# Optimization experiments

Hardware: AMD Instinct MI355X
Metric: run time of the kernel (lower is better)

## Reference

```python
import jax, jax.numpy as jnp
import numpy as np
import math

D_MODEL = 512
N_HEADS = 8
C = 1

def setup_inputs() -> dict:
    key = jax.random.key(0)
    ks = jax.random.split(key, 7)
    B, L, D = 4, 2048, 512
    f = lambda k, s: jax.random.normal(k, s, dtype=jnp.float32)
    return {
        "queries": f(ks[0], (B, L, D)),
        "keys": f(ks[1], (B, L, D)),
        "values": f(ks[2], (B, L, D)),
        "wq": f(ks[3], (D, D_MODEL)) * (1.0 / math.sqrt(D)),
        "wk": f(ks[4], (D, D_MODEL)) * (1.0 / math.sqrt(D)),
        "wv": f(ks[5], (D, D_MODEL)) * (1.0 / math.sqrt(D)),
        "wo": f(ks[6], (D_MODEL, D_MODEL)) * (1.0 / math.sqrt(D_MODEL)),
    }

def reference(queries, keys, values, wq, wk, wv, wo):
    B, Lq, _ = queries.shape
    Lk = keys.shape[1]
    H = N_HEADS
    Dh = D_MODEL // N_HEADS
    # projections -> [B,H,L,Dh]
    Q = (queries @ wq).reshape(B, Lq, H, Dh).transpose(0, 2, 1, 3)
    K = (keys @ wk).reshape(B, Lk, H, Dh).transpose(0, 2, 1, 3)
    V = (values @ wv).reshape(B, Lk, H, Dh).transpose(0, 2, 1, 3)
    # NOTE: original computes rfft/irfft correlation then OVERWRITES it with
    # this dense einsum; FFT branch is dead code and omitted here.
    corr = jnp.einsum('bhid,bhjd->bhij', Q, K)  # [B,H,Lq,Lk]
    # k derived from values.shape[3] == d_head in the original (quirk preserved)
    k = max(1, min(int(C * math.log(Dh)), Dh))
    mean_corr = corr.mean(axis=(1, 2))  # [B, Lk]
    top_vals, top_idx = jax.lax.top_k(mean_corr, k)  # [B,k]
    w = jax.nn.softmax(top_vals, axis=-1)  # [B,k]
    # rolled[b,j,h,l,d] = V[b,h,(l + delay[b,j]) % Lk, d]  (tf.roll with shift=-delay)
    idx = (jnp.arange(Lk)[None, None, :] + top_idx[:, :, None]) % Lk  # [B,k,Lk]
    gathered = jnp.take_along_axis(V[:, None], idx[:, :, None, :, None], axis=3)  # [B,k,H,Lk,Dh]
    agg = jnp.einsum('bk,bkhld->bhld', w, gathered)  # [B,H,Lk,Dh]
    # original: transpose (0,3,1,2) then reshape -> [B, Lq, d_model]
    out = agg.transpose(0, 3, 1, 2).reshape(B, Lq, D_MODEL)
    return out @ wo
```

## Files before the change

kernel.cpp:

```cpp
#include <hip/hip_runtime.h>
#include <hip/hip_bf16.h>
#include <float.h>
#include <math.h>

#define B  4
#define L  2048
#define D  512
#define K4 4

typedef __attribute__((ext_vector_type(8))) short  bf16x8;
typedef __attribute__((ext_vector_type(4))) float  f32x4;

#define VMIXB_OFF  0u
#define TT_OFF     8388608u
#define WVT_OFF    16777216u
#define WOT_OFF    17301504u
#define QPART_OFF  17825792u
#define TPART_OFF  18350080u
#define U_OFF      18415616u
#define SC_OFF     18423808u

static __device__ __forceinline__ unsigned short f2b(float f) {
    __hip_bfloat16 h = __float2bfloat16(f);
    return *reinterpret_cast<unsigned short*>(&h);
}

__global__ __launch_bounds__(256) void k_prep1(const float* __restrict__ q,
                                               const float* __restrict__ wv, const float* __restrict__ wo,
                                               float* __restrict__ qpart,
                                               unsigned short* __restrict__ wvT, unsigned short* __restrict__ woT) {
    __shared__ float s[32][33];
    int bid = blockIdx.x, tid = threadIdx.x;
    if (bid < 128) {
        int b = bid >> 5, lc = bid & 31;
        int c4 = tid & 127, half = tid >> 7;
        const float4* p = (const float4*)q + ((size_t)b * L + lc * 64 + half * 32) * 128 + c4;
        float4 a = make_float4(0.f, 0.f, 0.f, 0.f);
#pragma unroll 8
        for (int l = 0; l < 32; ++l) {
            float4 x = p[(size_t)l * 128];
            a.x += x.x; a.y += x.y; a.z += x.z; a.w += x.w;
        }
        ((float4*)qpart)[((b * 64) + lc * 2 + half) * 128 + c4] = a;
    } else {
        int id2 = bid - 128;
        int c0 = (id2 >> 4) * 32, n0 = (id2 & 15) * 32;
        int col = tid & 31, r8 = tid >> 5;
        for (int z = 0; z < 2; ++z) {
            const float* src = z ? wo : wv;
            unsigned short* dst = z ? woT : wvT;
#pragma unroll
            for (int rr = 0; rr < 4; ++rr) {
                int r = rr * 8 + r8;
                s[r][col] = src[(size_t)(c0 + r) * D + n0 + col];
            }
            __syncthreads();
#pragma unroll
            for (int rr = 0; rr < 4; ++rr) {
                int r = rr * 8 + r8;
                dst[(size_t)(n0 + r) * D + c0 + col] = f2b(s[col][r]);
            }
            __syncthreads();
        }
    }
}

__global__ void k_tpart(const float* __restrict__ wq, const float* __restrict__ qpart,
                        float* __restrict__ tpart) {
    __shared__ float part[256];
    __shared__ float qs[64];
    int b = blockIdx.x, jc = blockIdx.y, tid = threadIdx.x;
    int jj = tid & 63, cg = tid >> 6;
    float p = 0.f;
#pragma unroll
    for (int c = cg * 16; c < cg * 16 + 16; ++c)
        p += qpart[((b * 64) + c) * D + jc * 64 + jj];
    part[tid] = p;
    __syncthreads();
    if (tid < 64) qs[tid] = part[tid] + part[tid + 64] + part[tid + 128] + part[tid + 192];
    __syncthreads();
    float a0 = 0.f, a1 = 0.f;
#pragma unroll 8
    for (int j = 0; j < 64; ++j) {
        const float* wr = wq + (size_t)(jc * 64 + j) * D;
        float qv = qs[j];
        a0 += wr[tid] * qv;
        a1 += wr[tid + 256] * qv;
    }
    tpart[((b * 8) + jc) * D + tid] = a0;
    tpart[((b * 8) + jc) * D + tid + 256] = a1;
}

__global__ void k_uvec(const float* __restrict__ wk, const float* __restrict__ tpart,
                       float* __restrict__ u) {
    __shared__ __align__(16) float ts[D];
    int b = blockIdx.x, tid = threadIdx.x;
    for (int d = tid; d < D; d += 256) {
        float s = 0.f;
#pragma unroll
        for (int c = 0; c < 8; ++c) s += tpart[((b * 8) + c) * D + d];
        ts[d] = s;
    }
    __syncthreads();
    int wave = tid >> 6, lane = tid & 63;
    const float4* wk4 = (const float4*)wk;
    float4 t0 = *(const float4*)&ts[lane * 4];
    float4 t1 = *(const float4*)&ts[256 + lane * 4];
#pragma unroll
    for (int rr = 0; rr < 4; ++rr) {
        int i = blockIdx.y * 16 + wave * 4 + rr;
        float4 w0 = wk4[(size_t)i * 128 + lane];
        float4 w1 = wk4[(size_t)i * 128 + 64 + lane];
        float acc = w0.x * t0.x + w0.y * t0.y + w0.z * t0.z + w0.w * t0.w
                  + w1.x * t1.x + w1.y * t1.y + w1.z * t1.z + w1.w * t1.w;
        for (int m = 32; m; m >>= 1) acc += __shfl_xor(acc, m, 64);
        if (lane == 0) u[b * D + i] = acc * (1.f / 16384.f);
    }
}

__global__ void k_scores(const float* __restrict__ keys, const float* __restrict__ u,
                         float* __restrict__ sc) {
    __shared__ __align__(16) float us[D];
    int b = blockIdx.x, tid = threadIdx.x;
    for (int d = tid; d < D; d += 256) us[d] = u[b * D + d];
    __syncthreads();
    int wave = tid >> 6, lane = tid & 63;
    int j = blockIdx.y * 4 + wave;
    const float4* kp = (const float4*)(keys + ((size_t)b * L + j) * D);
    float4 u0 = *(const float4*)&us[lane * 4];
    float4 u1 = *(const float4*)&us[256 + lane * 4];
    float4 x0 = kp[lane], x1 = kp[lane + 64];
    float acc = x0.x * u0.x + x0.y * u0.y + x0.z * u0.z + x0.w * u0.w
              + x1.x * u1.x + x1.y * u1.y + x1.z * u1.z + x1.w * u1.w;
    for (int m = 32; m; m >>= 1) acc += __shfl_xor(acc, m, 64);
    if (lane == 0) sc[b * L + j] = acc;
}

__global__ __launch_bounds__(256) void k_vmixb(const float* __restrict__ values,
                                               const float* __restrict__ sc,
                                               uint4* __restrict__ vmixb) {
    __shared__ float sv[L];
    __shared__ float wv4[4]; __shared__ int wi4[4];
    __shared__ float wsh[K4]; __shared__ int ish[K4];
    int tid = threadIdx.x;
    int wave = tid >> 6, lane = tid & 63;
    int b = (int)(blockIdx.x >> 9);
    for (int i = tid; i < L; i += 256) sv[i] = sc[b * L + i];
    __syncthreads();
    float topv[K4]; int topi[K4];
    for (int it = 0; it < K4; ++it) {
        float bv = -FLT_MAX;
        int bi = 0x7fffffff;
#pragma unroll
        for (int i = 0; i < 8; ++i) {
            int idx = tid + i * 256;
            float v = sv[idx];
            if (v > bv) { bv = v; bi = idx; }
        }
        for (int m = 32; m; m >>= 1) {
            float v2 = __shfl_xor(bv, m, 64);
            int i2 = __shfl_xor(bi, m, 64);
            if (v2 > bv || (v2 == bv && i2 < bi)) { bv = v2; bi = i2; }
        }
        if (lane == 0) { wv4[wave] = bv; wi4[wave] = bi; }
        __syncthreads();
        float mv = wv4[0]; int mi = wi4[0];
#pragma unroll
        for (int w = 1; w < 4; ++w)
            if (wv4[w] > mv || (wv4[w] == mv && wi4[w] < mi)) { mv = wv4[w]; mi = wi4[w]; }
        topv[it] = mv; topi[it] = mi;
        if (tid == 0) sv[mi] = -FLT_MAX;
        __syncthreads();
    }
    if (tid == 0) {
        float mx = topv[0];
#pragma unroll
        for (int i = 1; i < K4; ++i) mx = fmaxf(mx, topv[i]);
        float ssum = 0.f, e[K4];
#pragma unroll
        for (int i = 0; i < K4; ++i) { e[i] = expf(topv[i] - mx); ssum += e[i]; }
#pragma unroll
        for (int i = 0; i < K4; ++i) { wsh[i] = e[i] / ssum; ish[i] = topi[i]; }
    }
    __syncthreads();

    size_t t = (size_t)blockIdx.x * 256 + tid;
    int l  = (int)((t >> 6) & (L - 1));
    int g8 = (int)(t & 63);
    const float4* vp = (const float4*)values;
    float4 r0 = make_float4(0.f, 0.f, 0.f, 0.f), r1 = r0;
#pragma unroll
    for (int j = 0; j < K4; ++j) {
        int ls = (l + ish[j]) & (L - 1);
        const float4* p = vp + ((size_t)b * L + ls) * 128 + g8 * 2;
        float4 x0 = p[0], x1 = p[1];
        float w = wsh[j];
        r0.x += w * x0.x; r0.y += w * x0.y; r0.z += w * x0.z; r0.w += w * x0.w;
        r1.x += w * x1.x; r1.y += w * x1.y; r1.z += w * x1.z; r1.w += w * x1.w;
    }
    uint4 o;
    o.x = (unsigned)f2b(r0.x) | ((unsigned)f2b(r0.y) << 16);
    o.y = (unsigned)f2b(r0.z) | ((unsigned)f2b(r0.w) << 16);
    o.z = (unsigned)f2b(r1.x) | ((unsigned)f2b(r1.y) << 16);
    o.w = (unsigned)f2b(r1.z) | ((unsigned)f2b(r1.w) << 16);
    vmixb[t] = o;
}

__global__ __launch_bounds__(256) void k_gemm1(const unsigned short* __restrict__ A,
                                               const unsigned short* __restrict__ Bt,
                                               unsigned short* __restrict__ Tt) {
    __shared__ __align__(16) unsigned short As[2][128][40];
    __shared__ __align__(16) unsigned short Bs[2][64][40];
    int m0 = blockIdx.x * 128, n0 = blockIdx.y * 64;
    int tid = threadIdx.x;
    int wave = tid >> 6, lane = tid & 63;
    int wr = wave >> 1, wc = wave & 1;
    int lr = lane & 15, lg = lane >> 4;
    f32x4 acc[4][2];
#pragma unroll
    for (int i = 0; i < 4; ++i)
#pragma unroll
        for (int j = 0; j < 2; ++j) acc[i][j] = (f32x4){0.f, 0.f, 0.f, 0.f};

    int aR = tid >> 1, aC = (tid & 1) * 16;
    int bR = tid >> 2, bC = (tid & 3) * 8;
    const unsigned short* Ap = A + (size_t)(m0 + aR) * D + aC;
    const unsigned short* Bp = Bt + (size_t)(n0 + bR) * D + bC;
    {
        uint4 va0 = *(const uint4*)(Ap);
        uint4 va1 = *(const uint4*)(Ap + 8);
        uint4 vb  = *(const uint4*)(Bp);
        *(uint4*)&As[0][aR][aC]     = va0;
        *(uint4*)&As[0][aR][aC + 8] = va1;
        *(uint4*)&Bs[0][bR][bC]     = vb;
    }
    __syncthreads();
    int cur = 0;
    for (int t = 0; t < 15; ++t) {
        int k0 = (t + 1) * 32;
        uint4 va0 = *(const uint4*)(Ap + k0);
        uint4 va1 = *(const uint4*)(Ap + k0 + 8);
        uint4 vb  = *(const uint4*)(Bp + k0);
        bf16x8 a[4], bq[2];
#pragma unroll
        for (int i = 0; i < 4; ++i) a[i] = *(const bf16x8*)&As[cur][wr * 64 + i * 16 + lr][lg * 8];
#pragma unroll
        for (int j = 0; j < 2; ++j) bq[j] = *(const bf16x8*)&Bs[cur][wc * 32 + j * 16 + lr][lg * 8];
#pragma unroll
        for (int i = 0; i < 4; ++i)
#pragma unroll
            for (int j = 0; j < 2; ++j)
                acc[i][j] = __builtin_amdgcn_mfma_f32_16x16x32_bf16(a[i], bq[j], acc[i][j], 0, 0, 0);
        *(uint4*)&As[cur ^ 1][aR][aC]     = va0;
        *(uint4*)&As[cur ^ 1][aR][aC + 8] = va1;
        *(uint4*)&Bs[cur ^ 1][bR][bC]     = vb;
        __syncthreads();
        cur ^= 1;
    }
    {
        bf16x8 a[4], bq[2];
#pragma unroll
        for (int i = 0; i < 4; ++i) a[i] = *(const bf16x8*)&As[cur][wr * 64 + i * 16 + lr][lg * 8];
#pragma unroll
        for (int j = 0; j < 2; ++j) bq[j] = *(const bf16x8*)&Bs[cur][wc * 32 + j * 16 + lr][lg * 8];
#pragma unroll
        for (int i = 0; i < 4; ++i)
#pragma unroll
            for (int j = 0; j < 2; ++j)
                acc[i][j] = __builtin_amdgcn_mfma_f32_16x16x32_bf16(a[i], bq[j], acc[i][j], 0, 0, 0);
    }
    int bb = m0 >> 11;
    int lbase = (m0 & (L - 1)) + wr * 64 + lg * 4;
#pragma unroll
    for (int i = 0; i < 4; ++i) {
        int lp = lbase + i * 16;
#pragma unroll
        for (int j = 0; j < 2; ++j) {
            int cn = n0 + wc * 32 + j * 16 + lr;
            uint2 pk;
            pk.x = (unsigned)f2b(acc[i][j][0]) | ((unsigned)f2b(acc[i][j][1]) << 16);
            pk.y = (unsigned)f2b(acc[i][j][2]) | ((unsigned)f2b(acc[i][j][3]) << 16);
            *(uint2*)&Tt[((size_t)bb * D + cn) * L + lp] = pk;
        }
    }
}

__global__ __launch_bounds__(256) void k_gemm2(const unsigned short* __restrict__ Tt,
                                               const unsigned short* __restrict__ Bt,
                                               float* __restrict__ out) {
    __shared__ __align__(16) unsigned short As[2][128][40];
    __shared__ __align__(16) unsigned short Bs[2][64][40];
    int m0 = blockIdx.x * 128, n0 = blockIdx.y * 64;
    int bs = blockIdx.z;
    int bb = bs >> 2, s = bs & 3;
    const unsigned short* Ab = Tt + (size_t)bb * D * L + (size_t)s * 512;
    int tid = threadIdx.x;
    int wave = tid >> 6, lane = tid & 63;
    int wr = wave >> 1, wc = wave & 1;
    int lr = lane & 15, lg = lane >> 4;
    f32x4 acc[4][2];
#pragma unroll
    for (int i = 0; i < 4; ++i)
#pragma unroll
        for (int j = 0; j < 2; ++j) acc[i][j] = (f32x4){0.f, 0.f, 0.f, 0.f};

    int aR = tid >> 1, aC = (tid & 1) * 16;
    int bR = tid >> 2, bC = (tid & 3) * 8;
    const unsigned short* Ap = Ab + (size_t)(m0 + aR) * L + aC;
    const unsigned short* Bp = Bt + (size_t)(n0 + bR) * D + bC;
    {
        uint4 va0 = *(const uint4*)(Ap);
        uint4 va1 = *(const uint4*)(Ap + 8);
        uint4 vb  = *(const uint4*)(Bp);
        *(uint4*)&As[0][aR][aC]     = va0;
        *(uint4*)&As[0][aR][aC + 8] = va1;
        *(uint4*)&Bs[0][bR][bC]     = vb;
    }
    __syncthreads();
    int cur = 0;
    for (int t = 0; t < 15; ++t) {
        int k0 = (t + 1) * 32;
        uint4 va0 = *(const uint4*)(Ap + k0);
        uint4 va1 = *(const uint4*)(Ap + k0 + 8);
        uint4 vb  = *(const uint4*)(Bp + k0);
        bf16x8 a[4], bq[2];
#pragma unroll
        for (int i = 0; i < 4; ++i) a[i] = *(const bf16x8*)&As[cur][wr * 64 + i * 16 + lr][lg * 8];
#pragma unroll
        for (int j = 0; j < 2; ++j) bq[j] = *(const bf16x8*)&Bs[cur][wc * 32 + j * 16 + lr][lg * 8];
#pragma unroll
        for (int i = 0; i < 4; ++i)
#pragma unroll
            for (int j = 0; j < 2; ++j)
                acc[i][j] = __builtin_amdgcn_mfma_f32_16x16x32_bf16(a[i], bq[j], acc[i][j], 0, 0, 0);
        *(uint4*)&As[cur ^ 1][aR][aC]     = va0;
        *(uint4*)&As[cur ^ 1][aR][aC + 8] = va1;
        *(uint4*)&Bs[cur ^ 1][bR][bC]     = vb;
        __syncthreads();
        cur ^= 1;
    }
    {
        bf16x8 a[4], bq[2];
#pragma unroll
        for (int i = 0; i < 4; ++i) a[i] = *(const bf16x8*)&As[cur][wr * 64 + i * 16 + lr][lg * 8];
#pragma unroll
        for (int j = 0; j < 2; ++j) bq[j] = *(const bf16x8*)&Bs[cur][wc * 32 + j * 16 + lr][lg * 8];
#pragma unroll
        for (int i = 0; i < 4; ++i)
#pragma unroll
            for (int j = 0; j < 2; ++j)
                acc[i][j] = __builtin_amdgcn_mfma_f32_16x16x32_bf16(a[i], bq[j], acc[i][j], 0, 0, 0);
    }
#pragma unroll
    for (int i = 0; i < 4; ++i) {
#pragma unroll
        for (int j = 0; j < 2; ++j) {
            int n = n0 + wc * 32 + j * 16 + lr;
#pragma unroll
            for (int r = 0; r < 4; ++r) {
                int m = m0 + wr * 64 + i * 16 + lg * 4 + r;
                int rr = ((m & 63) << 5) | ((m >> 6) << 2) | s;
                out[((size_t)bb * L + rr) * D + n] = acc[i][j][r];
            }
        }
    }
}

extern "C" void kernel_launch(void* const* d_in, const int* in_sizes, int n_in,
                              void* d_out, int out_size, void* d_ws, size_t ws_size,
                              hipStream_t stream) {
    const float* queries = (const float*)d_in[0];
    const float* keys    = (const float*)d_in[1];
    const float* values  = (const float*)d_in[2];
    const float* wq      = (const float*)d_in[3];
    const float* wk      = (const float*)d_in[4];
    const float* wv      = (const float*)d_in[5];
    const float* wo      = (const float*)d_in[6];
    float* out = (float*)d_out;
    char* ws = (char*)d_ws;

    unsigned short* vmixb = (unsigned short*)(ws + VMIXB_OFF);
    unsigned short* Tt    = (unsigned short*)(ws + TT_OFF);
    unsigned short* wvT   = (unsigned short*)(ws + WVT_OFF);
    unsigned short* woT   = (unsigned short*)(ws + WOT_OFF);
    float* qpart = (float*)(ws + QPART_OFF);
    float* tpart = (float*)(ws + TPART_OFF);
    float* u     = (float*)(ws + U_OFF);
    float* sc    = (float*)(ws + SC_OFF);

    k_prep1<<<384, 256, 0, stream>>>(queries, wv, wo, qpart, wvT, woT);
    k_tpart<<<dim3(B, 8), 256, 0, stream>>>(wq, qpart, tpart);
    k_uvec<<<dim3(B, 32), 256, 0, stream>>>(wk, tpart, u);
    k_scores<<<dim3(B, 512), 256, 0, stream>>>(keys, u, sc);
    k_vmixb<<<2048, 256, 0, stream>>>(values, sc, (uint4*)vmixb);
    k_gemm1<<<dim3(64, 8), 256, 0, stream>>>(vmixb, wvT, Tt);
    k_gemm2<<<dim3(4, 8, 16), 256, 0, stream>>>(Tt, woT, out);
}
```

Before: 67.22 us.

## Retile GEMM operands into K-blocked layout and stage via direct global-to-LDS loads

Producers (weight transpose, value mixing, gemm1 epilogue) now write bf16 operands in a K-blocked [kblock][row][32] layout, so each 128x32 or 64x32 tile is contiguous in memory. Both GEMMs then fetch tiles with global_load_lds 16-byte loads straight into shared memory, skipping the register round trip and the explicit LDS stores. The LDS row padding is removed to match the contiguous copy, which may bring back bank conflicts on the MFMA fragment reads. The producers' write patterns also change, which may affect their coalescing.

```diff
diff --git a/kernel.cpp b/kernel.cpp
--- a/kernel.cpp
+++ b/kernel.cpp
@@ -23,6 +23,12 @@
 static __device__ __forceinline__ unsigned short f2b(float f) {
     __hip_bfloat16 h = __float2bfloat16(f);
     return *reinterpret_cast<unsigned short*>(&h);
+}
+
+static __device__ __forceinline__ void gload16(const void* g, void* l) {
+    __builtin_amdgcn_global_load_lds(
+        (__attribute__((address_space(1))) void*)(g),
+        (__attribute__((address_space(3))) void*)(l), 16, 0, 0);
 }
 
 __global__ __launch_bounds__(256) void k_prep1(const float* __restrict__ q,
@@ -45,6 +51,7 @@
     } else {
         int id2 = bid - 128;
         int c0 = (id2 >> 4) * 32, n0 = (id2 & 15) * 32;
+        int kb = c0 >> 5;
         int col = tid & 31, r8 = tid >> 5;
         for (int z = 0; z < 2; ++z) {
             const float* src = z ? wo : wv;
@@ -58,7 +65,7 @@
 #pragma unroll
             for (int rr = 0; rr < 4; ++rr) {
                 int r = rr * 8 + r8;
-                dst[(size_t)(n0 + r) * D + c0 + col] = f2b(s[col][r]);
+                dst[((size_t)kb * 512 + n0 + r) * 32 + col] = f2b(s[col][r]);
             }
             __syncthreads();
         }
@@ -138,13 +145,14 @@
 
 __global__ __launch_bounds__(256) void k_vmixb(const float* __restrict__ values,
                                                const float* __restrict__ sc,
-                                               uint4* __restrict__ vmixb) {
+                                               unsigned short* __restrict__ vmixb) {
     __shared__ float sv[L];
     __shared__ float wv4[4]; __shared__ int wi4[4];
     __shared__ float wsh[K4]; __shared__ int ish[K4];
     int tid = threadIdx.x;
     int wave = tid >> 6, lane = tid & 63;
-    int b = (int)(blockIdx.x >> 9);
+    int bid = blockIdx.x;
+    int b = bid >> 9;
     for (int i = tid; i < L; i += 256) sv[i] = sc[b * L + i];
     __syncthreads();
     float topv[K4]; int topi[K4];
@@ -184,15 +192,15 @@
     }
     __syncthreads();
 
-    size_t t = (size_t)blockIdx.x * 256 + tid;
-    int l  = (int)((t >> 6) & (L - 1));
-    int g8 = (int)(t & 63);
+    int kb = (bid >> 5) & 15;
+    int l  = (bid & 31) * 64 + (tid >> 2);
+    int ko = (tid & 3) * 8;
     const float4* vp = (const float4*)values;
     float4 r0 = make_float4(0.f, 0.f, 0.f, 0.f), r1 = r0;
 #pragma unroll
     for (int j = 0; j < K4; ++j) {
         int ls = (l + ish[j]) & (L - 1);
-        const float4* p = vp + ((size_t)b * L + ls) * 128 + g8 * 2;
+        const float4* p = vp + ((size_t)b * L + ls) * 128 + kb * 8 + (tid & 3) * 2;
         float4 x0 = p[0], x1 = p[1];
         float w = wsh[j];
         r0.x += w * x0.x; r0.y += w * x0.y; r0.z += w * x0.z; r0.w += w * x0.w;
@@ -203,15 +211,17 @@
     o.y = (unsigned)f2b(r0.z) | ((unsigned)f2b(r0.w) << 16);
     o.z = (unsigned)f2b(r1.x) | ((unsigned)f2b(r1.y) << 16);
     o.w = (unsigned)f2b(r1.z) | ((unsigned)f2b(r1.w) << 16);
-    vmixb[t] = o;
+    size_t off = ((size_t)(b * 16 + kb) * 2048 + l) * 32 + ko;
+    *(uint4*)(vmixb + off) = o;
 }
 
 __global__ __launch_bounds__(256) void k_gemm1(const unsigned short* __restrict__ A,
                                                const unsigned short* __restrict__ Bt,
                                                unsigned short* __restrict__ Tt) {
-    __shared__ __align__(16) unsigned short As[2][128][40];
-    __shared__ __align__(16) unsigned short Bs[2][64][40];
+    __shared__ __align__(16) unsigned short As[2][128][32];
+    __shared__ __align__(16) unsigned short Bs[2][64][32];
     int m0 = blockIdx.x * 128, n0 = blockIdx.y * 64;
+    int b = m0 >> 11, ml = m0 & (L - 1);
     int tid = threadIdx.x;
     int wave = tid >> 6, lane = tid & 63;
     int wr = wave >> 1, wc = wave & 1;
@@ -222,25 +232,25 @@
 #pragma unroll
         for (int j = 0; j < 2; ++j) acc[i][j] = (f32x4){0.f, 0.f, 0.f, 0.f};
 
-    int aR = tid >> 1, aC = (tid & 1) * 16;
-    int bR = tid >> 2, bC = (tid & 3) * 8;
-    const unsigned short* Ap = A + (size_t)(m0 + aR) * D + aC;
-    const unsigned short* Bp = Bt + (size_t)(n0 + bR) * D + bC;
-    {
-        uint4 va0 = *(const uint4*)(Ap);
-        uint4 va1 = *(const uint4*)(Ap + 8);
-        uint4 vb  = *(const uint4*)(Bp);
-        *(uint4*)&As[0][aR][aC]     = va0;
-        *(uint4*)&As[0][aR][aC + 8] = va1;
-        *(uint4*)&Bs[0][bR][bC]     = vb;
-    }
+    int lbyte = tid * 16;
+    int wbase = (tid >> 6) * 1024;
+
+#define STAGE1(buf, kb)                                                                   \
+    {                                                                                     \
+        const char* gA = (const char*)(A + ((size_t)(b * 16 + (kb)) * 2048 + ml) * 32);   \
+        const char* gB = (const char*)(Bt + ((size_t)(kb) * 512 + n0) * 32);              \
+        char* lA = ((char*)&As[buf][0][0]) + wbase;                                       \
+        char* lB = ((char*)&Bs[buf][0][0]) + wbase;                                       \
+        gload16(gA + lbyte, lA);                                                          \
+        gload16(gA + 4096 + lbyte, lA + 4096);                                            \
+        gload16(gB + lbyte, lB);                                                          \
+    }
+
+    STAGE1(0, 0);
     __syncthreads();
     int cur = 0;
     for (int t = 0; t < 15; ++t) {
-        int k0 = (t + 1) * 32;
-        uint4 va0 = *(const uint4*)(Ap + k0);
-        uint4 va1 = *(const uint4*)(Ap + k0 + 8);
-        uint4 vb  = *(const uint4*)(Bp + k0);
+        STAGE1(cur ^ 1, t + 1);
         bf16x8 a[4], bq[2];
 #pragma unroll
         for (int i = 0; i < 4; ++i) a[i] = *(const bf16x8*)&As[cur][wr * 64 + i * 16 + lr][lg * 8];
@@ -251,9 +261,6 @@
 #pragma unroll
             for (int j = 0; j < 2; ++j)
                 acc[i][j] = __builtin_amdgcn_mfma_f32_16x16x32_bf16(a[i], bq[j], acc[i][j], 0, 0, 0);
-        *(uint4*)&As[cur ^ 1][aR][aC]     = va0;
-        *(uint4*)&As[cur ^ 1][aR][aC + 8] = va1;
-        *(uint4*)&Bs[cur ^ 1][bR][bC]     = vb;
         __syncthreads();
         cur ^= 1;
     }
@@ -269,18 +276,18 @@
             for (int j = 0; j < 2; ++j)
                 acc[i][j] = __builtin_amdgcn_mfma_f32_16x16x32_bf16(a[i], bq[j], acc[i][j], 0, 0, 0);
     }
-    int bb = m0 >> 11;
-    int lbase = (m0 & (L - 1)) + wr * 64 + lg * 4;
+#undef STAGE1
 #pragma unroll
     for (int i = 0; i < 4; ++i) {
-        int lp = lbase + i * 16;
+        int lglob = ml + wr * 64 + i * 16 + lg * 4;
+        int ls = lglob >> 5, lo = lglob & 31;
 #pragma unroll
         for (int j = 0; j < 2; ++j) {
             int cn = n0 + wc * 32 + j * 16 + lr;
             uint2 pk;
             pk.x = (unsigned)f2b(acc[i][j][0]) | ((unsigned)f2b(acc[i][j][1]) << 16);
             pk.y = (unsigned)f2b(acc[i][j][2]) | ((unsigned)f2b(acc[i][j][3]) << 16);
-            *(uint2*)&Tt[((size_t)bb * D + cn) * L + lp] = pk;
+            *(uint2*)&Tt[((size_t)(b * 64 + ls) * 512 + cn) * 32 + lo] = pk;
         }
     }
 }
@@ -288,12 +295,11 @@
 __global__ __launch_bounds__(256) void k_gemm2(const unsigned short* __restrict__ Tt,
                                                const unsigned short* __restrict__ Bt,
                                                float* __restrict__ out) {
-    __shared__ __align__(16) unsigned short As[2][128][40];
-    __shared__ __align__(16) unsigned short Bs[2][64][40];
+    __shared__ __align__(16) unsigned short As[2][128][32];
+    __shared__ __align__(16) unsigned short Bs[2][64][32];
     int m0 = blockIdx.x * 128, n0 = blockIdx.y * 64;
     int bs = blockIdx.z;
     int bb = bs >> 2, s = bs & 3;
-    const unsigned short* Ab = Tt + (size_t)bb * D * L + (size_t)s * 512;
     int tid = threadIdx.x;
     int wave = tid >> 6, lane = tid & 63;
     int wr = wave >> 1, wc = wave & 1;
@@ -304,25 +310,25 @@
 #pragma unroll
         for (int j = 0; j < 2; ++j) acc[i][j] = (f32x4){0.f, 0.f, 0.f, 0.f};
 
-    int aR = tid >> 1, aC = (tid & 1) * 16;
-    int bR = tid >> 2, bC = (tid & 3) * 8;
-    const unsigned short* Ap = Ab + (size_t)(m0 + aR) * L + aC;
-    const unsigned short* Bp = Bt + (size_t)(n0 + bR) * D + bC;
-    {
-        uint4 va0 = *(const uint4*)(Ap);
-        uint4 va1 = *(const uint4*)(Ap + 8);
-        uint4 vb  = *(const uint4*)(Bp);
-        *(uint4*)&As[0][aR][aC]     = va0;
-        *(uint4*)&As[0][aR][aC + 8] = va1;
-        *(uint4*)&Bs[0][bR][bC]     = vb;
-    }
+    int lbyte = tid * 16;
+    int wbase = (tid >> 6) * 1024;
+
+#define STAGE2(buf, t)                                                                        \
+    {                                                                                         \
+        const char* gA = (const char*)(Tt + ((size_t)(bb * 64 + s * 16 + (t)) * 512 + m0) * 32); \
+        const char* gB = (const char*)(Bt + ((size_t)(t) * 512 + n0) * 32);                   \
+        char* lA = ((char*)&As[buf][0][0]) + wbase;                                           \
+        char* lB = ((char*)&Bs[buf][0][0]) + wbase;                                           \
+        gload16(gA + lbyte, lA);                                                              \
+        gload16(gA + 4096 + lbyte, lA + 4096);                                                \
+        gload16(gB + lbyte, lB);                                                              \
+    }
+
+    STAGE2(0, 0);
     __syncthreads();
     int cur = 0;
     for (int t = 0; t < 15; ++t) {
-        int k0 = (t + 1) * 32;
-        uint4 va0 = *(const uint4*)(Ap + k0);
-        uint4 va1 = *(const uint4*)(Ap + k0 + 8);
-        uint4 vb  = *(const uint4*)(Bp + k0);
+        STAGE2(cur ^ 1, t + 1);
         bf16x8 a[4], bq[2];
 #pragma unroll
         for (int i = 0; i < 4; ++i) a[i] = *(const bf16x8*)&As[cur][wr * 64 + i * 16 + lr][lg * 8];
@@ -333,9 +339,6 @@
 #pragma unroll
             for (int j = 0; j < 2; ++j)
                 acc[i][j] = __builtin_amdgcn_mfma_f32_16x16x32_bf16(a[i], bq[j], acc[i][j], 0, 0, 0);
-        *(uint4*)&As[cur ^ 1][aR][aC]     = va0;
-        *(uint4*)&As[cur ^ 1][aR][aC + 8] = va1;
-        *(uint4*)&Bs[cur ^ 1][bR][bC]     = vb;
         __syncthreads();
         cur ^= 1;
     }
@@ -351,6 +354,7 @@
             for (int j = 0; j < 2; ++j)
                 acc[i][j] = __builtin_amdgcn_mfma_f32_16x16x32_bf16(a[i], bq[j], acc[i][j], 0, 0, 0);
     }
+#undef STAGE2
 #pragma unroll
     for (int i = 0; i < 4; ++i) {
 #pragma unroll
@@ -392,7 +396,7 @@
     k_tpart<<<dim3(B, 8), 256, 0, stream>>>(wq, qpart, tpart);
     k_uvec<<<dim3(B, 32), 256, 0, stream>>>(wk, tpart, u);
     k_scores<<<dim3(B, 512), 256, 0, stream>>>(keys, u, sc);
-    k_vmixb<<<2048, 256, 0, stream>>>(values, sc, (uint4*)vmixb);
+    k_vmixb<<<2048, 256, 0, stream>>>(values, sc, vmixb);
     k_gemm1<<<dim3(64, 8), 256, 0, stream>>>(vmixb, wvT, Tt);
     k_gemm2<<<dim3(4, 8, 16), 256, 0, stream>>>(Tt, woT, out);
 }
```

Result: slower. 69.25 us (+3.0%).
